# Kernel tuning notes

Hardware: AMD Instinct MI355X
Metric: run time of the kernel (lower is better)

Reference implementation:

```python
import jax, jax.numpy as jnp
import numpy as np


def setup_inputs() -> dict:
    key = jax.random.key(0)
    kq, kk, kv = jax.random.split(key, 3)
    B, L, H, E = 4, 2048, 16, 64
    return {
        "queries": jax.random.normal(kq, (B, L, H, E), dtype=jnp.float32),
        "keys": jax.random.normal(kk, (B, L, H, E), dtype=jnp.float32),
        "values": jax.random.normal(kv, (B, L, H, E), dtype=jnp.float32),
    }


def reference(queries, keys, values):
    # queries: [B,L,H,E], keys: [B,S,H,E], values: [B,S,H,D]
    B, L, H, E = queries.shape
    S = keys.shape[1]
    scale = 1.0 / jnp.sqrt(jnp.asarray(E, dtype=queries.dtype))
    scores = jnp.einsum("blhe,bshe->bhls", queries, keys)  # [B,H,L,S]
    # causal mask: block strictly-upper-triangular (future) positions
    causal = jnp.tril(jnp.ones((L, S), dtype=bool))  # True = keep
    scores = jnp.where(causal[None, None, :, :], scores, -jnp.inf)
    A = jax.nn.softmax(scale * scores, axis=-1)  # dropout p=0 -> identity
    V = jnp.einsum("bhls,bshd->blhd", A, values)
    return V
```

## Files before the change

kernel.cpp:

```cpp
#include <hip/hip_runtime.h>
#include <hip/hip_bf16.h>

typedef float f32x4 __attribute__((ext_vector_type(4)));
typedef __bf16 bf16x8 __attribute__((ext_vector_type(8)));
typedef unsigned short u16x8 __attribute__((ext_vector_type(8)));
typedef unsigned short u16x4 __attribute__((ext_vector_type(4)));
typedef unsigned u32x4 __attribute__((ext_vector_type(4)));

#define NB 4
#define SL 2048
#define NH 16
#define HD 64
#define KBLK 64
#define PAD 72
#define NT 16

static __device__ __forceinline__ unsigned short f2bf(float f) {
    unsigned u = __builtin_bit_cast(unsigned, f);
    u += 0x7fffu + ((u >> 16) & 1u);
    return (unsigned short)(u >> 16);
}

static __device__ __forceinline__ unsigned pk2(float lo, float hi) {
    unsigned r;
    asm("v_cvt_pk_bf16_f32 %0, %1, %2" : "=v"(r) : "v"(lo), "v"(hi));
    return r;
}

static __device__ __forceinline__ float fexp2(float x) {
    float r;
    asm("v_exp_f32 %0, %1" : "=v"(r) : "v"(x));
    return r;
}

static __device__ __forceinline__ void pl32swap(unsigned& a, unsigned& b) {
    asm("v_permlane32_swap_b32 %0, %1" : "+v"(a), "+v"(b));
}
static __device__ __forceinline__ void pl16swap(unsigned& a, unsigned& b) {
    asm("v_permlane16_swap_b32 %0, %1" : "+v"(a), "+v"(b));
}

__global__ void conv_k(const float* __restrict__ Kg, unsigned short* __restrict__ Kb) {
    const int idx = (blockIdx.x * 256 + threadIdx.x) * 4;
    const int e    = idx & 63;
    const int rest = idx >> 6;
    const int h    = rest & 15;
    const int bs   = rest >> 4;
    const int b    = bs >> 11;
    const int s    = bs & (SL - 1);
    f32x4 v = *(const f32x4*)(Kg + idx);
    u16x4 o;
    #pragma unroll
    for (int j = 0; j < 4; ++j) o[j] = f2bf(v[j]);
    *(u16x4*)(Kb + (((size_t)(b * NH + h) * SL + s) * HD + e)) = o;
}

__global__ void conv_v(const float* __restrict__ Vg, unsigned short* __restrict__ Vtb) {
    __shared__ unsigned short T[64 * PAD];
    const int tid = threadIdx.x;
    const int id  = blockIdx.x;
    const int st  = id & 31;
    const int bh  = id >> 5;
    const int s0  = st * 64;
    {
        const int sl = tid >> 2, c = (tid & 3) * 16;
        const float* src = Vg + ((size_t)((bh >> 4) * SL + s0 + sl) * NH + (bh & 15)) * HD + c;
        u16x8 a, b2;
        #pragma unroll
        for (int j = 0; j < 8; ++j) { a[j] = f2bf(src[j]); b2[j] = f2bf(src[8 + j]); }
        *(u16x8*)&T[sl * PAD + c]     = a;
        *(u16x8*)&T[sl * PAD + c + 8] = b2;
    }
    __syncthreads();
    {
        const int d = tid >> 2, sc = (tid & 3) * 16;
        u16x8 o0, o1;
        #pragma unroll
        for (int j = 0; j < 8; ++j) { o0[j] = T[(sc + j) * PAD + d]; o1[j] = T[(sc + 8 + j) * PAD + d]; }
        unsigned short* dst = Vtb + ((size_t)bh * HD + d) * SL + s0 + sc;
        *(u16x8*)dst       = o0;
        *(u16x8*)(dst + 8) = o1;
    }
}

__global__ __launch_bounds__(256, 2)
void fattn_kernel(const float* __restrict__ Qg, const unsigned short* __restrict__ Kb,
                  const unsigned short* __restrict__ Vtb, float* __restrict__ Og)
{
    __shared__ unsigned short Klds[KBLK * PAD];
    __shared__ unsigned short Vlds[HD * PAD];

    const int tid  = threadIdx.x;
    const int w    = tid >> 6;
    const int lane = tid & 63;
    const int g    = lane >> 4;
    const int li   = lane & 15;

    const int bh   = blockIdx.x & 63;
    const int rawp = blockIdx.x >> 6;
    const int p    = (rawp < 4) ? rawp : 11 - rawp;
    const int b    = bh >> 4;
    const int h    = bh & 15;

    int qrows[4];
    qrows[0] = p * 128 + w * 16;
    qrows[1] = p * 128 + 64 + w * 16;
    qrows[2] = (NT - 1 - p) * 128 + w * 16;
    qrows[3] = (NT - 1 - p) * 128 + 64 + w * 16;
    const int tmax = 2 * (NT - 1 - p) + 1;

    const float QSCALE = 0.125f * 1.44269504088896f;
    bf16x8 qfrag[4][2];
    #pragma unroll
    for (int fi = 0; fi < 4; ++fi) {
        const int q = qrows[fi] + li;
        const float* qp = Qg + ((size_t)(b * SL + q) * NH + h) * HD + g * 8;
        #pragma unroll
        for (int c = 0; c < 2; ++c) {
            f32x4 a = *(const f32x4*)(qp + c * 32);
            f32x4 b2 = *(const f32x4*)(qp + c * 32 + 4);
            u16x8 t;
            #pragma unroll
            for (int j = 0; j < 4; ++j) { t[j] = f2bf(a[j] * QSCALE); t[4 + j] = f2bf(b2[j] * QSCALE); }
            qfrag[fi][c] = __builtin_bit_cast(bf16x8, t);
        }
    }

    float m_run[4] = {-1e30f, -1e30f, -1e30f, -1e30f};
    float l_run[4] = {0.f, 0.f, 0.f, 0.f};
    f32x4 oacc[4][4];
    #pragma unroll
    for (int fi = 0; fi < 4; ++fi)
        #pragma unroll
        for (int d = 0; d < 4; ++d) oacc[fi][d] = f32x4{0.f, 0.f, 0.f, 0.f};

    const int srow = tid >> 2;
    const int scol = (tid & 3) * 16;
    const unsigned short* kbase = Kb  + (size_t)bh * SL * HD;
    const unsigned short* vbase = Vtb + (size_t)bh * HD * SL;

    u16x8 kr0 = *(const u16x8*)(kbase + (size_t)srow * HD + scol);
    u16x8 kr1 = *(const u16x8*)(kbase + (size_t)srow * HD + scol + 8);
    u16x8 vr0 = *(const u16x8*)(vbase + (size_t)srow * SL + scol);
    u16x8 vr1 = *(const u16x8*)(vbase + (size_t)srow * SL + scol + 8);

    for (int t = 0; t <= tmax; ++t) {
        const int s0 = t * KBLK;
        __syncthreads();
        *(u16x8*)&Klds[srow * PAD + scol]     = kr0;
        *(u16x8*)&Klds[srow * PAD + scol + 8] = kr1;
        *(u16x8*)&Vlds[srow * PAD + scol]     = vr0;
        *(u16x8*)&Vlds[srow * PAD + scol + 8] = vr1;
        if (t < tmax) {
            const int s1 = s0 + KBLK;
            kr0 = *(const u16x8*)(kbase + ((size_t)(s1 + srow)) * HD + scol);
            kr1 = *(const u16x8*)(kbase + ((size_t)(s1 + srow)) * HD + scol + 8);
            vr0 = *(const u16x8*)(vbase + (size_t)srow * SL + s1 + scol);
            vr1 = *(const u16x8*)(vbase + (size_t)srow * SL + s1 + scol + 8);
        }
        __syncthreads();

        bool act[4];
        #pragma unroll
        for (int fi = 0; fi < 4; ++fi) act[fi] = (s0 <= qrows[fi] + 15);

        bf16x8 kfr[4][2];
        #pragma unroll
        for (int sub = 0; sub < 4; ++sub) {
            kfr[sub][0] = __builtin_bit_cast(bf16x8, *(u16x8*)&Klds[(sub * 16 + li) * PAD + g * 8]);
            kfr[sub][1] = __builtin_bit_cast(bf16x8, *(u16x8*)&Klds[(sub * 16 + li) * PAD + 32 + g * 8]);
        }

        bf16x8 pfr[4][2];
        #pragma unroll
        for (int fi = 0; fi < 4; ++fi) {
            if (!act[fi]) continue;
            const int qf = qrows[fi];

            f32x4 sacc[4];
            #pragma unroll
            for (int sub = 0; sub < 4; ++sub) {
                f32x4 c = f32x4{0.f, 0.f, 0.f, 0.f};
                c = __builtin_amdgcn_mfma_f32_16x16x32_bf16(kfr[sub][0], qfrag[fi][0], c, 0, 0, 0);
                c = __builtin_amdgcn_mfma_f32_16x16x32_bf16(kfr[sub][1], qfrag[fi][1], c, 0, 0, 0);
                sacc[sub] = c;
            }

            if (s0 + KBLK - 1 > qf) {
                const int q = qf + li;
                #pragma unroll
                for (int sub = 0; sub < 4; ++sub)
                    #pragma unroll
                    for (int r = 0; r < 4; ++r)
                        if (s0 + sub * 16 + g * 4 + r > q) sacc[sub][r] = -1e30f;
            }

            float pmax = sacc[0][0];
            #pragma unroll
            for (int sub = 0; sub < 4; ++sub)
                #pragma unroll
                for (int r = 0; r < 4; ++r) pmax = fmaxf(pmax, sacc[sub][r]);
            pmax = fmaxf(pmax, __shfl_xor(pmax, 16, 64));
            pmax = fmaxf(pmax, __shfl_xor(pmax, 32, 64));

            if (!__all(pmax - m_run[fi] <= 8.0f)) {
                const float mnew = fmaxf(m_run[fi], pmax);
                const float alpha = fexp2(m_run[fi] - mnew);
                m_run[fi] = mnew;
                l_run[fi] *= alpha;
                #pragma unroll
                for (int d = 0; d < 4; ++d)
                    #pragma unroll
                    for (int r = 0; r < 4; ++r) oacc[fi][d][r] *= alpha;
            }

            float rsum = 0.f;
            #pragma unroll
            for (int sub = 0; sub < 4; ++sub)
                #pragma unroll
                for (int r = 0; r < 4; ++r) {
                    const float pv = fexp2(sacc[sub][r] - m_run[fi]);
                    sacc[sub][r] = pv;
                    rsum += pv;
                }
            rsum += __shfl_xor(rsum, 16, 64);
            rsum += __shfl_xor(rsum, 32, 64);
            l_run[fi] += rsum;

            unsigned X00 = pk2(sacc[0][0], sacc[0][1]);
            unsigned X01 = pk2(sacc[0][2], sacc[0][3]);
            unsigned X10 = pk2(sacc[1][0], sacc[1][1]);
            unsigned X11 = pk2(sacc[1][2], sacc[1][3]);
            unsigned X20 = pk2(sacc[2][0], sacc[2][1]);
            unsigned X21 = pk2(sacc[2][2], sacc[2][3]);
            unsigned X30 = pk2(sacc[3][0], sacc[3][1]);
            unsigned X31 = pk2(sacc[3][2], sacc[3][3]);
            pl32swap(X00, X10); pl16swap(X00, X10);
            pl32swap(X01, X11); pl16swap(X01, X11);
            pl32swap(X20, X30); pl16swap(X20, X30);
            pl32swap(X21, X31); pl16swap(X21, X31);
            u32x4 w0 = {X00, X01, X10, X11};
            u32x4 w1 = {X20, X21, X30, X31};
            pfr[fi][0] = __builtin_bit_cast(bf16x8, w0);
            pfr[fi][1] = __builtin_bit_cast(bf16x8, w1);
        }

        #pragma unroll
        for (int d = 0; d < 4; ++d) {
            bf16x8 vf0 = __builtin_bit_cast(bf16x8, *(u16x8*)&Vlds[(d * 16 + li) * PAD + g * 8]);
            bf16x8 vf1 = __builtin_bit_cast(bf16x8, *(u16x8*)&Vlds[(d * 16 + li) * PAD + 32 + g * 8]);
            #pragma unroll
            for (int fi = 0; fi < 4; ++fi) {
                if (!act[fi]) continue;
                oacc[fi][d] = __builtin_amdgcn_mfma_f32_16x16x32_bf16(vf0, pfr[fi][0], oacc[fi][d], 0, 0, 0);
                oacc[fi][d] = __builtin_amdgcn_mfma_f32_16x16x32_bf16(vf1, pfr[fi][1], oacc[fi][d], 0, 0, 0);
            }
        }
    }

    #pragma unroll
    for (int fi = 0; fi < 4; ++fi) {
        const float inv = 1.0f / l_run[fi];
        float* op = Og + ((size_t)(b * SL + qrows[fi] + li) * NH + h) * HD + g * 4;
        #pragma unroll
        for (int d = 0; d < 4; ++d) {
            f32x4 o = oacc[fi][d];
            #pragma unroll
            for (int r = 0; r < 4; ++r) o[r] *= inv;
            *(f32x4*)(op + d * 16) = o;
        }
    }
}

extern "C" void kernel_launch(void* const* d_in, const int* in_sizes, int n_in,
                              void* d_out, int out_size, void* d_ws, size_t ws_size,
                              hipStream_t stream) {
    const float* Qg = (const float*)d_in[0];
    const float* Kg = (const float*)d_in[1];
    const float* Vg = (const float*)d_in[2];
    float* Og = (float*)d_out;

    const size_t elems = (size_t)NB * NH * SL * HD;
    if (ws_size < 2 * elems * sizeof(unsigned short)) return;
    unsigned short* Kb  = (unsigned short*)d_ws;
    unsigned short* Vtb = Kb + elems;

    hipLaunchKernelGGL(conv_k, dim3(elems / 4 / 256), dim3(256), 0, stream, Kg, Kb);
    hipLaunchKernelGGL(conv_v, dim3(NB * NH * (SL / 64)), dim3(256), 0, stream, Vg, Vtb);
    hipLaunchKernelGGL(fattn_kernel, dim3(8 * 64), dim3(256), 0, stream,
                       Qg, Kb, Vtb, Og);
}
```

Baseline: 91.20 us.

## Fuse K bf16 conversion into attention kernel and defer row-sum reduction

Removes the separate K conversion kernel and its workspace. The attention kernel now loads fp32 K straight from the original layout and packs it to bf16 before writing to LDS. It also replaces the serial max and sum reductions with tree reductions, and defers the cross-lane row-sum shuffles to the epilogue. This saves one launch and a full K write-plus-read pass, at the cost of doubling K global-load bytes per block and adding conversion work inside the main loop.

```diff
diff --git a/kernel.cpp b/kernel.cpp
--- a/kernel.cpp
+++ b/kernel.cpp
@@ -38,21 +38,6 @@
 }
 static __device__ __forceinline__ void pl16swap(unsigned& a, unsigned& b) {
     asm("v_permlane16_swap_b32 %0, %1" : "+v"(a), "+v"(b));
-}
-
-__global__ void conv_k(const float* __restrict__ Kg, unsigned short* __restrict__ Kb) {
-    const int idx = (blockIdx.x * 256 + threadIdx.x) * 4;
-    const int e    = idx & 63;
-    const int rest = idx >> 6;
-    const int h    = rest & 15;
-    const int bs   = rest >> 4;
-    const int b    = bs >> 11;
-    const int s    = bs & (SL - 1);
-    f32x4 v = *(const f32x4*)(Kg + idx);
-    u16x4 o;
-    #pragma unroll
-    for (int j = 0; j < 4; ++j) o[j] = f2bf(v[j]);
-    *(u16x4*)(Kb + (((size_t)(b * NH + h) * SL + s) * HD + e)) = o;
 }
 
 __global__ void conv_v(const float* __restrict__ Vg, unsigned short* __restrict__ Vtb) {
@@ -84,7 +69,7 @@
 }
 
 __global__ __launch_bounds__(256, 2)
-void fattn_kernel(const float* __restrict__ Qg, const unsigned short* __restrict__ Kb,
+void fattn_kernel(const float* __restrict__ Qg, const float* __restrict__ Kg,
                   const unsigned short* __restrict__ Vtb, float* __restrict__ Og)
 {
     __shared__ unsigned short Klds[KBLK * PAD];
@@ -136,25 +121,37 @@
 
     const int srow = tid >> 2;
     const int scol = (tid & 3) * 16;
-    const unsigned short* kbase = Kb  + (size_t)bh * SL * HD;
+    const float* kgbase = Kg + ((size_t)b * SL * NH + h) * HD;
     const unsigned short* vbase = Vtb + (size_t)bh * HD * SL;
 
-    u16x8 kr0 = *(const u16x8*)(kbase + (size_t)srow * HD + scol);
-    u16x8 kr1 = *(const u16x8*)(kbase + (size_t)srow * HD + scol + 8);
+    f32x4 kf[4];
+    #pragma unroll
+    for (int j = 0; j < 4; ++j)
+        kf[j] = *(const f32x4*)(kgbase + (size_t)srow * NH * HD + scol + j * 4);
     u16x8 vr0 = *(const u16x8*)(vbase + (size_t)srow * SL + scol);
     u16x8 vr1 = *(const u16x8*)(vbase + (size_t)srow * SL + scol + 8);
 
     for (int t = 0; t <= tmax; ++t) {
         const int s0 = t * KBLK;
         __syncthreads();
-        *(u16x8*)&Klds[srow * PAD + scol]     = kr0;
-        *(u16x8*)&Klds[srow * PAD + scol + 8] = kr1;
-        *(u16x8*)&Vlds[srow * PAD + scol]     = vr0;
-        *(u16x8*)&Vlds[srow * PAD + scol + 8] = vr1;
+        {
+            u16x8 kw0, kw1;
+            u32x4 a0 = {pk2(kf[0][0], kf[0][1]), pk2(kf[0][2], kf[0][3]),
+                        pk2(kf[1][0], kf[1][1]), pk2(kf[1][2], kf[1][3])};
+            u32x4 a1 = {pk2(kf[2][0], kf[2][1]), pk2(kf[2][2], kf[2][3]),
+                        pk2(kf[3][0], kf[3][1]), pk2(kf[3][2], kf[3][3])};
+            kw0 = __builtin_bit_cast(u16x8, a0);
+            kw1 = __builtin_bit_cast(u16x8, a1);
+            *(u16x8*)&Klds[srow * PAD + scol]     = kw0;
+            *(u16x8*)&Klds[srow * PAD + scol + 8] = kw1;
+            *(u16x8*)&Vlds[srow * PAD + scol]     = vr0;
+            *(u16x8*)&Vlds[srow * PAD + scol + 8] = vr1;
+        }
         if (t < tmax) {
             const int s1 = s0 + KBLK;
-            kr0 = *(const u16x8*)(kbase + ((size_t)(s1 + srow)) * HD + scol);
-            kr1 = *(const u16x8*)(kbase + ((size_t)(s1 + srow)) * HD + scol + 8);
+            #pragma unroll
+            for (int j = 0; j < 4; ++j)
+                kf[j] = *(const f32x4*)(kgbase + (size_t)(s1 + srow) * NH * HD + scol + j * 4);
             vr0 = *(const u16x8*)(vbase + (size_t)srow * SL + s1 + scol);
             vr1 = *(const u16x8*)(vbase + (size_t)srow * SL + s1 + scol + 8);
         }
@@ -195,11 +192,12 @@
                         if (s0 + sub * 16 + g * 4 + r > q) sacc[sub][r] = -1e30f;
             }
 
-            float pmax = sacc[0][0];
-            #pragma unroll
-            for (int sub = 0; sub < 4; ++sub)
-                #pragma unroll
-                for (int r = 0; r < 4; ++r) pmax = fmaxf(pmax, sacc[sub][r]);
+            float a0 = fmaxf(sacc[0][0], sacc[0][1]), a1 = fmaxf(sacc[0][2], sacc[0][3]);
+            float a2 = fmaxf(sacc[1][0], sacc[1][1]), a3 = fmaxf(sacc[1][2], sacc[1][3]);
+            float a4 = fmaxf(sacc[2][0], sacc[2][1]), a5 = fmaxf(sacc[2][2], sacc[2][3]);
+            float a6 = fmaxf(sacc[3][0], sacc[3][1]), a7 = fmaxf(sacc[3][2], sacc[3][3]);
+            float b0 = fmaxf(a0, a1), b1 = fmaxf(a2, a3), b2 = fmaxf(a4, a5), b3 = fmaxf(a6, a7);
+            float pmax = fmaxf(fmaxf(b0, b1), fmaxf(b2, b3));
             pmax = fmaxf(pmax, __shfl_xor(pmax, 16, 64));
             pmax = fmaxf(pmax, __shfl_xor(pmax, 32, 64));
 
@@ -214,18 +212,16 @@
                     for (int r = 0; r < 4; ++r) oacc[fi][d][r] *= alpha;
             }
 
-            float rsum = 0.f;
             #pragma unroll
             for (int sub = 0; sub < 4; ++sub)
                 #pragma unroll
-                for (int r = 0; r < 4; ++r) {
-                    const float pv = fexp2(sacc[sub][r] - m_run[fi]);
-                    sacc[sub][r] = pv;
-                    rsum += pv;
-                }
-            rsum += __shfl_xor(rsum, 16, 64);
-            rsum += __shfl_xor(rsum, 32, 64);
-            l_run[fi] += rsum;
+                for (int r = 0; r < 4; ++r)
+                    sacc[sub][r] = fexp2(sacc[sub][r] - m_run[fi]);
+            float s0a = (sacc[0][0] + sacc[0][1]) + (sacc[0][2] + sacc[0][3]);
+            float s1a = (sacc[1][0] + sacc[1][1]) + (sacc[1][2] + sacc[1][3]);
+            float s2a = (sacc[2][0] + sacc[2][1]) + (sacc[2][2] + sacc[2][3]);
+            float s3a = (sacc[3][0] + sacc[3][1]) + (sacc[3][2] + sacc[3][3]);
+            l_run[fi] += (s0a + s1a) + (s2a + s3a);
 
             unsigned X00 = pk2(sacc[0][0], sacc[0][1]);
             unsigned X01 = pk2(sacc[0][2], sacc[0][3]);
@@ -260,7 +256,10 @@
 
     #pragma unroll
     for (int fi = 0; fi < 4; ++fi) {
-        const float inv = 1.0f / l_run[fi];
+        float lt = l_run[fi];
+        lt += __shfl_xor(lt, 16, 64);
+        lt += __shfl_xor(lt, 32, 64);
+        const float inv = 1.0f / lt;
         float* op = Og + ((size_t)(b * SL + qrows[fi] + li) * NH + h) * HD + g * 4;
         #pragma unroll
         for (int d = 0; d < 4; ++d) {
@@ -281,12 +280,10 @@
     float* Og = (float*)d_out;
 
     const size_t elems = (size_t)NB * NH * SL * HD;
-    if (ws_size < 2 * elems * sizeof(unsigned short)) return;
-    unsigned short* Kb  = (unsigned short*)d_ws;
-    unsigned short* Vtb = Kb + elems;
-
-    hipLaunchKernelGGL(conv_k, dim3(elems / 4 / 256), dim3(256), 0, stream, Kg, Kb);
+    if (ws_size < elems * sizeof(unsigned short)) return;
+    unsigned short* Vtb = (unsigned short*)d_ws;
+
     hipLaunchKernelGGL(conv_v, dim3(NB * NH * (SL / 64)), dim3(256), 0, stream, Vg, Vtb);
     hipLaunchKernelGGL(fattn_kernel, dim3(8 * 64), dim3(256), 0, stream,
-                       Qg, Kb, Vtb, Og);
-}
+                       Qg, Kg, Vtb, Og);
+}
```

Result: faster. 83.00 us (-9.0%).
